# Optimization experiments

Measured on AMD Instinct MI355X. Metric: run time of the kernel, lower is better.

## Reference

```python
import jax, jax.numpy as jnp
import numpy as np

B, L, H = 4096, 4096, 1024  # batch, num_labels, hidden_size


def setup_inputs() -> dict:
    key = jax.random.key(0)
    k1, k2, k3, k4, k5 = jax.random.split(key, 5)
    return {
        "bert_output": jax.random.normal(k1, (B, H), dtype=jnp.float32),
        "label_embed": jax.random.normal(k2, (L, H), dtype=jnp.float32),
        "W": jax.random.normal(k3, (L, H), dtype=jnp.float32) * 0.02,
        "b": jax.random.normal(k4, (L,), dtype=jnp.float32) * 0.02,
        "labels": jax.random.randint(k5, (B, L), 0, 2, dtype=jnp.int32),
    }


def reference(bert_output, label_embed, W, b, labels):
    # Original: output[i, j] = classifier(bert_output[i] + label_embed[j])[j]
    #         = sum_k (x[i,k] + E[j,k]) * W[j,k] + b[j]
    #         = (x @ W^T)[i,j] + (E * W).sum(-1)[j] + b[j]
    xWt = jnp.einsum('bh,lh->bl', bert_output, W)          # [B, L] GEMM
    diag_bias = jnp.sum(label_embed * W, axis=-1) + b       # [L] epilogue
    logits = xWt + diag_bias[None, :]                       # [B, L]
    return logits
```

## Files before the change

kernel.cpp:

```cpp
#include <hip/hip_runtime.h>
#include <hip/hip_bf16.h>

#define Bdim 4096
#define Ldim 4096
#define Hdim 1024
#define BM 256
#define BN 256
#define BK 64
#define NT (Hdim / BK)

typedef __attribute__((ext_vector_type(8))) __bf16 bf16x8;
typedef __attribute__((ext_vector_type(4))) float floatx4;

__device__ __forceinline__ unsigned short f2bf(float f) {
  union { __hip_bfloat16 h; unsigned short u; } c;
  c.h = __float2bfloat16(f);
  return c.u;
}

__global__ __launch_bounds__(256) void prep_kernel(
    const float* __restrict__ X, const float* __restrict__ E,
    const float* __restrict__ W, const float* __restrict__ b,
    unsigned short* __restrict__ Xb, unsigned short* __restrict__ Wb,
    float* __restrict__ bias) {
  const int blk = blockIdx.x;
  const int t = threadIdx.x;
  if (blk < Ldim) {
    const int row = blk;
    const float4 wv = reinterpret_cast<const float4*>(W + (size_t)row * Hdim)[t];
    const float4 ev = reinterpret_cast<const float4*>(E + (size_t)row * Hdim)[t];
    ushort4 o;
    o.x = f2bf(wv.x); o.y = f2bf(wv.y); o.z = f2bf(wv.z); o.w = f2bf(wv.w);
    reinterpret_cast<ushort4*>(Wb + (size_t)row * Hdim)[t] = o;
    float dot = wv.x * ev.x + wv.y * ev.y + wv.z * ev.z + wv.w * ev.w;
#pragma unroll
    for (int off = 32; off > 0; off >>= 1) dot += __shfl_down(dot, off, 64);
    __shared__ float part[4];
    if ((t & 63) == 0) part[t >> 6] = dot;
    __syncthreads();
    if (t == 0) bias[row] = part[0] + part[1] + part[2] + part[3] + b[row];
  } else {
    const int i = (blk - Ldim) * 256 + t;
    float4 v = reinterpret_cast<const float4*>(X)[i];
    ushort4 o;
    o.x = f2bf(v.x); o.y = f2bf(v.y); o.z = f2bf(v.z); o.w = f2bf(v.w);
    reinterpret_cast<ushort4*>(Xb)[i] = o;
  }
}

__global__ __launch_bounds__(512, 2) void gemm_bias_kernel(
    const unsigned short* __restrict__ A,
    const unsigned short* __restrict__ Bw,
    const float* __restrict__ bias,
    float* __restrict__ C) {
  static_assert(NT >= 3, "pipeline needs >=3 K-tiles");
  __shared__ __align__(16) unsigned short lds[2][2][BM * BK];

  const int tid = threadIdx.x;
  const int wave = tid >> 6;
  const int lane = tid & 63;
  const int wm = wave >> 2;
  const int wn = wave & 3;
  const int m_blk = blockIdx.y * BM;
  const int n_blk = blockIdx.x * BN;

  const int srow = wave * 8 + (lane >> 3);
  const int skofs = ((lane & 7) ^ (lane >> 3)) * 8;
  const unsigned short* gA = A + (size_t)(m_blk + srow) * Hdim + skofs;
  const unsigned short* gB = Bw + (size_t)(n_blk + srow) * Hdim + skofs;

  const int fr = lane & 15;
  const int fq = lane >> 4;
  const int kx0 = ((fq) ^ (fr & 7)) * 8;
  const int kx1 = ((4 + fq) ^ (fr & 7)) * 8;
  const int aBase = (wm * 128 + fr) * BK;
  const int bBase = (wn * 64 + fr) * BK;

  floatx4 acc[8][4] = {};
  bf16x8 af[8][2], bfv[4][2];

#define GLL(src, dst)                                                  \
  __builtin_amdgcn_global_load_lds(                                    \
      (const __attribute__((address_space(1))) void*)(src),            \
      (__attribute__((address_space(3))) void*)(dst), 16, 0, 0)

#define STAGE1(c, mat, j, kt)                                          \
  do {                                                                 \
    const unsigned short* _g = (mat) ? gB : gA;                        \
    GLL(_g + (size_t)((j) * 128) * Hdim + (size_t)(kt) * 64,           \
        &lds[c][mat][((j) * 128 + wave * 8) * BK]);                    \
    GLL(_g + (size_t)((j) * 128 + 64) * Hdim + (size_t)(kt) * 64,      \
        &lds[c][mat][((j) * 128 + 64 + wave * 8) * BK]);               \
  } while (0)

#define READ_A(c, lo)                                                  \
  do {                                                                 \
    _Pragma("unroll") for (int mi = (lo); mi < (lo) + 4; ++mi) {       \
      af[mi][0] = *(const bf16x8*)&lds[c][0][aBase + mi * 16 * BK + kx0]; \
      af[mi][1] = *(const bf16x8*)&lds[c][0][aBase + mi * 16 * BK + kx1]; \
    }                                                                  \
  } while (0)

#define READ_B(c, lo)                                                  \
  do {                                                                 \
    _Pragma("unroll") for (int ni = (lo); ni < (lo) + 2; ++ni) {       \
      bfv[ni][0] = *(const bf16x8*)&lds[c][1][bBase + ni * 16 * BK + kx0]; \
      bfv[ni][1] = *(const bf16x8*)&lds[c][1][bBase + ni * 16 * BK + kx1]; \
    }                                                                  \
  } while (0)

#define MFMA_Q(M0, N0)                                                 \
  do {                                                                 \
    __builtin_amdgcn_s_setprio(1);                                     \
    _Pragma("unroll") for (int mi = (M0); mi < (M0) + 4; ++mi)         \
      _Pragma("unroll") for (int ni = (N0); ni < (N0) + 2; ++ni) {     \
        acc[mi][ni] = __builtin_amdgcn_mfma_f32_16x16x32_bf16(         \
            af[mi][0], bfv[ni][0], acc[mi][ni], 0, 0, 0);              \
        acc[mi][ni] = __builtin_amdgcn_mfma_f32_16x16x32_bf16(         \
            af[mi][1], bfv[ni][1], acc[mi][ni], 0, 0, 0);              \
      }                                                                \
    __builtin_amdgcn_s_setprio(0);                                     \
  } while (0)

#define BAR __builtin_amdgcn_s_barrier()
#define LGKM0 asm volatile("s_waitcnt lgkmcnt(0)" ::: "memory")

  STAGE1(0, 0, 0, 0);
  STAGE1(0, 0, 1, 0);
  STAGE1(0, 1, 0, 0);
  STAGE1(0, 1, 1, 0);
  STAGE1(1, 0, 0, 1);
  asm volatile("s_waitcnt vmcnt(2)\n\ts_barrier" ::: "memory");

#pragma unroll 1
  for (int t = 0; t < NT - 1; ++t) {
    const int c = t & 1;
    STAGE1(c ^ 1, 0, 1, t + 1);
    STAGE1(c ^ 1, 1, 0, t + 1);
    READ_A(c, 0);
    READ_B(c, 0);
    BAR;
    LGKM0;
    MFMA_Q(0, 0);
    BAR;
    STAGE1(c ^ 1, 1, 1, t + 1);
    READ_A(c, 4);
    BAR;
    LGKM0;
    MFMA_Q(4, 0);
    BAR;
    READ_B(c, 2);
    BAR;
    LGKM0;
    MFMA_Q(0, 2);
    BAR;
    if (t < NT - 2) {
      STAGE1(c, 0, 0, t + 2);
      asm volatile("s_waitcnt vmcnt(2)\n\ts_barrier" ::: "memory");
    } else {
      asm volatile("s_waitcnt vmcnt(0)\n\ts_barrier" ::: "memory");
    }
    MFMA_Q(4, 2);
    BAR;
  }

  READ_A(1, 0);
  READ_B(1, 0);
  READ_A(1, 4);
  READ_B(1, 2);
  LGKM0;
  MFMA_Q(0, 0);
  MFMA_Q(4, 0);
  MFMA_Q(0, 2);
  MFMA_Q(4, 2);

#undef GLL
#undef STAGE1
#undef READ_A
#undef READ_B
#undef MFMA_Q
#undef BAR
#undef LGKM0

  const int col0 = n_blk + wn * 64 + fr;
  const int row0 = m_blk + wm * 128 + fq * 4;
#pragma unroll
  for (int ni = 0; ni < 4; ++ni) {
    const float bs = bias[col0 + ni * 16];
#pragma unroll
    for (int mi = 0; mi < 8; ++mi) {
      float* cp = C + (size_t)(row0 + mi * 16) * Ldim + (col0 + ni * 16);
      floatx4 v = acc[mi][ni];
      cp[0 * (size_t)Ldim] = v.x + bs;
      cp[1 * (size_t)Ldim] = v.y + bs;
      cp[2 * (size_t)Ldim] = v.z + bs;
      cp[3 * (size_t)Ldim] = v.w + bs;
    }
  }
}

extern "C" void kernel_launch(void* const* d_in, const int* in_sizes, int n_in,
                              void* d_out, int out_size, void* d_ws, size_t ws_size,
                              hipStream_t stream) {
  const float* X = (const float*)d_in[0];
  const float* E = (const float*)d_in[1];
  const float* W = (const float*)d_in[2];
  const float* b = (const float*)d_in[3];
  float* out = (float*)d_out;

  unsigned short* Xb = (unsigned short*)d_ws;
  unsigned short* Wb = Xb + (size_t)Bdim * Hdim;
  float* bias = (float*)(Wb + (size_t)Ldim * Hdim);

  prep_kernel<<<Ldim + Bdim, 256, 0, stream>>>(X, E, W, b, Xb, Wb, bias);
  dim3 grid(Ldim / BN, Bdim / BM);
  gemm_bias_kernel<<<grid, 512, 0, stream>>>(Xb, Wb, bias, out);
}
```

Baseline: 55.79 us.

## Restructure GEMM K-loop pipeline to prefetch A two tiles ahead

Reworks the software pipeline of the bf16 MFMA GEMM. The A operand for tile k+2 is now staged into the current LDS buffer after its last read, and B for tile k+1 is staged into the other buffer, with gating at vmcnt(4). The loop is unrolled by two with compile-time buffer indices, and the trailing barrier of each tile is dropped. The goal is more global-load latency hiding and less barrier and index overhead. In exchange it keeps more loads in flight, and the barrier reasoning is subtler, which raises the risk of LDS hazards.

```diff
diff --git a/kernel.cpp b/kernel.cpp
--- a/kernel.cpp
+++ b/kernel.cpp
@@ -53,7 +53,6 @@
     const unsigned short* __restrict__ Bw,
     const float* __restrict__ bias,
     float* __restrict__ C) {
-  static_assert(NT >= 3, "pipeline needs >=3 K-tiles");
   __shared__ __align__(16) unsigned short lds[2][2][BM * BK];
 
   const int tid = threadIdx.x;
@@ -84,13 +83,13 @@
       (const __attribute__((address_space(1))) void*)(src),            \
       (__attribute__((address_space(3))) void*)(dst), 16, 0, 0)
 
-#define STAGE1(c, mat, j, kt)                                          \
+#define STAGE_H(c, mat, h, kt)                                         \
   do {                                                                 \
     const unsigned short* _g = (mat) ? gB : gA;                        \
-    GLL(_g + (size_t)((j) * 128) * Hdim + (size_t)(kt) * 64,           \
-        &lds[c][mat][((j) * 128 + wave * 8) * BK]);                    \
-    GLL(_g + (size_t)((j) * 128 + 64) * Hdim + (size_t)(kt) * 64,      \
-        &lds[c][mat][((j) * 128 + 64 + wave * 8) * BK]);               \
+    GLL(_g + (size_t)((h) * 128) * Hdim + (size_t)(kt) * BK,           \
+        &lds[c][mat][((h) * 128 + wave * 8) * BK]);                    \
+    GLL(_g + (size_t)((h) * 128 + 64) * Hdim + (size_t)(kt) * BK,      \
+        &lds[c][mat][((h) * 128 + 64 + wave * 8) * BK]);               \
   } while (0)
 
 #define READ_A(c, lo)                                                  \
@@ -124,63 +123,61 @@
 
 #define BAR __builtin_amdgcn_s_barrier()
 #define LGKM0 asm volatile("s_waitcnt lgkmcnt(0)" ::: "memory")
-
-  STAGE1(0, 0, 0, 0);
-  STAGE1(0, 0, 1, 0);
-  STAGE1(0, 1, 0, 0);
-  STAGE1(0, 1, 1, 0);
-  STAGE1(1, 0, 0, 1);
-  asm volatile("s_waitcnt vmcnt(2)\n\ts_barrier" ::: "memory");
+#define GATE4 asm volatile("s_waitcnt vmcnt(4)\n\ts_barrier" ::: "memory")
+#define GATE0 asm volatile("s_waitcnt vmcnt(0)\n\ts_barrier" ::: "memory")
+
+#define TILE_BODY(c, o, kt, DO_B, DO_A, GATE)                          \
+  do {                                                                 \
+                                                               \
+    if (DO_B) STAGE_H(o, 1, 0, (kt) + 1);                              \
+    READ_A(c, 0);                                                      \
+    READ_B(c, 0);                                                      \
+    BAR; LGKM0;                                                        \
+    MFMA_Q(0, 0);                                                      \
+                                                               \
+    if (DO_B) STAGE_H(o, 1, 1, (kt) + 1);                              \
+    READ_A(c, 4);                                                      \
+    BAR; LGKM0;                                                        \
+    MFMA_Q(4, 0);                                                      \
+    BAR;   \
+                                                               \
+    if (DO_A) STAGE_H(c, 0, 0, (kt) + 2);                              \
+    READ_B(c, 2);                                                      \
+    BAR; LGKM0;                                                        \
+    MFMA_Q(0, 2);                                                      \
+    BAR;                  \
+                                                               \
+    if (DO_A) STAGE_H(c, 0, 1, (kt) + 2);                              \
+    GATE;                                                              \
+    MFMA_Q(4, 2);                                                      \
+  } while (0)
+
+  STAGE_H(0, 0, 0, 0);
+  STAGE_H(0, 0, 1, 0);
+  STAGE_H(0, 1, 0, 0);
+  STAGE_H(0, 1, 1, 0);
+  STAGE_H(1, 0, 0, 1);
+  STAGE_H(1, 0, 1, 1);
+  GATE4;
 
 #pragma unroll 1
-  for (int t = 0; t < NT - 1; ++t) {
-    const int c = t & 1;
-    STAGE1(c ^ 1, 0, 1, t + 1);
-    STAGE1(c ^ 1, 1, 0, t + 1);
-    READ_A(c, 0);
-    READ_B(c, 0);
-    BAR;
-    LGKM0;
-    MFMA_Q(0, 0);
-    BAR;
-    STAGE1(c ^ 1, 1, 1, t + 1);
-    READ_A(c, 4);
-    BAR;
-    LGKM0;
-    MFMA_Q(4, 0);
-    BAR;
-    READ_B(c, 2);
-    BAR;
-    LGKM0;
-    MFMA_Q(0, 2);
-    BAR;
-    if (t < NT - 2) {
-      STAGE1(c, 0, 0, t + 2);
-      asm volatile("s_waitcnt vmcnt(2)\n\ts_barrier" ::: "memory");
-    } else {
-      asm volatile("s_waitcnt vmcnt(0)\n\ts_barrier" ::: "memory");
-    }
-    MFMA_Q(4, 2);
-    BAR;
+  for (int t = 0; t < NT - 2; t += 2) {
+    TILE_BODY(0, 1, t, 1, 1, GATE4);
+    TILE_BODY(1, 0, t + 1, 1, 1, GATE4);
   }
-
-  READ_A(1, 0);
-  READ_B(1, 0);
-  READ_A(1, 4);
-  READ_B(1, 2);
-  LGKM0;
-  MFMA_Q(0, 0);
-  MFMA_Q(4, 0);
-  MFMA_Q(0, 2);
-  MFMA_Q(4, 2);
+  TILE_BODY(0, 1, NT - 2, 1, 0, GATE0);
+  TILE_BODY(1, 0, NT - 1, 0, 0, (void)0);
 
 #undef GLL
-#undef STAGE1
+#undef STAGE_H
 #undef READ_A
 #undef READ_B
 #undef MFMA_Q
 #undef BAR
 #undef LGKM0
+#undef GATE4
+#undef GATE0
+#undef TILE_BODY
 
   const int col0 = n_blk + wn * 64 + fr;
   const int row0 = m_blk + wm * 128 + fq * 4;
```

Result: faster. 50.23 us (-10.0%).
